# Kernel tuning notes

Hardware: AMD Instinct MI355X
Metric: run time of the kernel (lower is better)

The kernel has to match this reference:

```python
import jax, jax.numpy as jnp
import numpy as np

B, N, D, DB, C = 1024, 131072, 256, 512, 96


def setup_inputs() -> dict:
    key = jax.random.key(0)
    ks = jax.random.split(key, 9)
    s1 = 1.0 / np.sqrt(D)   # torch Linear default init bound for W1/b1
    s2 = 1.0 / np.sqrt(DB)  # for W2
    sl = 1.0 / np.sqrt(2.0) # custom init for label Linear(1, D)
    return {
        "x": jax.random.normal(ks[0], (B, D), jnp.float32),
        "k": jax.random.normal(ks[1], (B, D), jnp.float32),
        "candidate_k": jax.random.normal(ks[2], (N, D), jnp.float32),
        "candidate_y": jax.random.normal(ks[3], (N,), jnp.float32),
        "W_lbl": jax.random.uniform(ks[4], (D, 1), jnp.float32, -sl, sl),
        "b_lbl": jax.random.uniform(ks[5], (D,), jnp.float32, -sl, sl),
        "W1": jax.random.uniform(ks[6], (DB, D), jnp.float32, -s1, s1),
        "b1": jax.random.uniform(ks[7], (DB,), jnp.float32, -s1, s1),
        "W2": jax.random.uniform(ks[8], (D, DB), jnp.float32, -s2, s2),
        "context_size": C,
    }


def reference(x, k, candidate_k, candidate_y, W_lbl, b_lbl, W1, b1, W2, context_size):
    # --- exact L2 kNN search (FAISS IndexFlatL2 equivalent, eval path) ---
    # argmin_c ||k - c||^2 == argmax_c (2 k.c - ||c||^2); ||k||^2 is constant per row.
    neg_dist = 2.0 * (k @ candidate_k.T) - jnp.sum(candidate_k * candidate_k, axis=-1)[None, :]  # [B, N]
    _, context_idx = jax.lax.top_k(neg_dist, context_size)  # [B, C], non-differentiable (matches torch.no_grad)

    context_k = candidate_k[context_idx]  # [B, C, D]
    context_y = candidate_y[context_idx]  # [B, C]

    # similarities = -||k||^2 + 2 k.ck - ||ck||^2
    sim = (-jnp.sum(k * k, axis=-1, keepdims=True)
           + 2.0 * jnp.einsum('bd,bcd->bc', k, context_k)
           - jnp.sum(context_k * context_k, axis=-1))
    probs = jax.nn.softmax(sim, axis=-1)  # context_dropout=0 -> identity

    # label_encoder = Linear(1, D): y[..., None] @ W_lbl.T + b_lbl
    context_y_emb = context_y[..., None] * W_lbl[:, 0] + b_lbl  # [B, C, D]

    # T = Linear(D, DB) -> ReLU -> (dropout0=0) -> Linear(DB, D, bias=False)
    diff = k[:, None, :] - context_k                            # [B, C, D]
    h = jax.nn.relu(jnp.einsum('bcd,ed->bce', diff, W1) + b1)   # [B, C, DB]
    values = context_y_emb + jnp.einsum('bce,de->bcd', h, W2)   # [B, C, D]

    context_x = jnp.einsum('bc,bcd->bd', probs, values)
    return x + context_x
```

## Files before the change

kernel.cpp:

```cpp
#include <hip/hip_runtime.h>
#include <stdint.h>

#define B_   1024
#define N_   131072
#define D_   256
#define DB_  512
#define C_   96
#define CAP_ 2048

#define CHUNK_   4096
#define TILE_SH_ 32768

typedef __attribute__((ext_vector_type(8))) short bf16x8;
typedef __attribute__((ext_vector_type(4))) float f32x4;

__device__ __forceinline__ unsigned short f2bf(float x) {
  union { float f; unsigned u; } v; v.f = x;
  unsigned r = v.u + 0x7FFFu + ((v.u >> 16) & 1u);
  return (unsigned short)(r >> 16);
}
__device__ __forceinline__ float bf2f(unsigned short b) {
  union { unsigned u; float f; } v; v.u = ((unsigned)b) << 16;
  return v.f;
}

#if __has_builtin(__builtin_amdgcn_global_load_lds)
#define USE_ASYNC_LDS 1
#else
#define USE_ASYNC_LDS 0
#endif

__device__ __forceinline__ void stage_chunk(const unsigned short* chunk,
                                            unsigned short* lds, int t) {
#if USE_ASYNC_LDS
  char* base = (char*)lds + (t >> 6) * 1024;
  const unsigned short* g0 = chunk + t * 8;
  __builtin_amdgcn_global_load_lds((__attribute__((address_space(1))) void*)g0,
                                   (__attribute__((address_space(3))) void*)base, 16, 0, 0);
  __builtin_amdgcn_global_load_lds((__attribute__((address_space(1))) void*)(g0 + 2048),
                                   (__attribute__((address_space(3))) void*)(base + 4096), 16, 0, 0);
#else
  *(uint4*)((char*)lds + t * 16)        = *(const uint4*)(chunk + t * 8);
  *(uint4*)((char*)lds + t * 16 + 4096) = *(const uint4*)(chunk + t * 8 + 2048);
#endif
}

__global__ __launch_bounds__(256) void k_prep_cand(const float* __restrict__ cand,
                                                   unsigned short* __restrict__ cand_bf,
                                                   float* __restrict__ cnorm) {
  int w = threadIdx.x >> 6, l = threadIdx.x & 63;
  int row = blockIdx.x * 4 + w;
  float4 v = ((const float4*)(cand + (size_t)row * D_))[l];
  float s = v.x * v.x + v.y * v.y + v.z * v.z + v.w * v.w;
  ushort4 o = make_ushort4(f2bf(v.x), f2bf(v.y), f2bf(v.z), f2bf(v.w));
  int nt = row >> 7, r = row & 127;
  int kkc = l >> 3, cin = (l & 7) * 4;
  int c = (((cin >> 3) ^ ((r >> 1) & 3)) << 3) | (cin & 7);
  *(ushort4*)(cand_bf + ((size_t)nt * 8 + kkc) * CHUNK_ + r * 32 + c) = o;
  for (int off = 32; off; off >>= 1) s += __shfl_down(s, off);
  if (l == 0) cnorm[row] = s;
}

__global__ __launch_bounds__(256) void k_prep_k(const float* __restrict__ k,
                                                const float* __restrict__ W1,
                                                const float* __restrict__ b1,
                                                unsigned short* __restrict__ k_bf,
                                                float* __restrict__ knorm,
                                                float* __restrict__ tau,
                                                float* __restrict__ aprime) {
  __shared__ __align__(16) float kb[D_];
  __shared__ float red[4];
  int t = threadIdx.x, b = blockIdx.x;
  float kv = k[(size_t)b * D_ + t];
  kb[t] = kv;
  {
    int mt = b >> 7, r = b & 127;
    int kkc = t >> 5, cin = t & 31;
    int cb = (cin >> 3) ^ ((r >> 1) & 3);
    int c = (cb << 3) | (cin & 7);
    k_bf[((size_t)mt * 8 + kkc) * CHUNK_ + r * 32 + c] = f2bf(kv);
  }
  float p = kv * kv;
  for (int off = 32; off; off >>= 1) p += __shfl_down(p, off);
  if ((t & 63) == 0) red[t >> 6] = p;
  __syncthreads();
  if (t == 0) {
    float kn = red[0] + red[1] + red[2] + red[3];
    knorm[b] = kn;
    tau[b] = -256.0f + 2.5f * sqrtf(4.0f * kn + 512.0f);
  }
  for (int e = t; e < DB_; e += 256) {
    const float4* wr = (const float4*)(W1 + (size_t)e * D_);
    const float4* k4 = (const float4*)kb;
    float acc = 0.f;
    #pragma unroll 8
    for (int d = 0; d < D_ / 4; ++d) {
      float4 wv = wr[d], kv4 = k4[d];
      acc += wv.x * kv4.x + wv.y * kv4.y + wv.z * kv4.z + wv.w * kv4.w;
    }
    aprime[(size_t)b * DB_ + e] = acc + b1[e];
  }
}

__global__ __launch_bounds__(256) void k_prep_w1(const float* __restrict__ W1,
                                                 unsigned short* __restrict__ w1bf) {
  int i = blockIdx.x * 256 + threadIdx.x;
  float4 v = ((const float4*)W1)[i];
  int e = i >> 6, f4 = i & 63;
  int d0 = f4 * 4;
  int nt = e >> 7, r = e & 127;
  int kkc = d0 >> 5, cin = d0 & 31;
  int cb = (cin >> 3) ^ ((r >> 1) & 3);
  int c = (cb << 3) | (cin & 7);
  *(ushort4*)(w1bf + ((size_t)nt * 8 + kkc) * CHUNK_ + r * 32 + c) =
      make_ushort4(f2bf(v.x), f2bf(v.y), f2bf(v.z), f2bf(v.w));
}

__global__ __launch_bounds__(256, 2) void k_score(const unsigned short* __restrict__ k_bf,
                                                  const unsigned short* __restrict__ cand_bf,
                                                  const float* __restrict__ cnorm,
                                                  const float* __restrict__ tau,
                                                  unsigned* __restrict__ count,
                                                  int* __restrict__ l_idx,
                                                  float* __restrict__ l_s) {
  __shared__ __align__(16) unsigned short As[2][CHUNK_];
  __shared__ __align__(16) unsigned short Bs[2][CHUNK_];
  __shared__ float tauS[128], cnS[128];
  int t = threadIdx.x;
  unsigned x = blockIdx.x;
  unsigned xcd = x & 7u, j = x >> 3;
  int mt = (int)(j & 7u), nt = (int)(xcd + ((j >> 3) << 3));
  int m0 = mt * 128, n0 = nt * 128;
  const unsigned short* Ag = k_bf + (size_t)mt * TILE_SH_;
  const unsigned short* Bg = cand_bf + (size_t)nt * TILE_SH_;
  if (t < 128) tauS[t] = tau[m0 + t];
  if (t < 128) cnS[t] = cnorm[n0 + t];
  int lane = t & 63, w = t >> 6;
  int mb = (w & 1) * 64, nb = (w >> 1) * 64;
  int fr = lane & 15, fk = (lane >> 4) * 8;
  int fsw = fk ^ (((fr >> 1) & 3) << 3);
  f32x4 acc[4][4] = {};
  stage_chunk(Ag, As[0], t);
  stage_chunk(Bg, Bs[0], t);
  __syncthreads();
  #pragma unroll
  for (int kkc = 0; kkc < 8; ++kkc) {
    int cur = kkc & 1;
    if (kkc < 7) {
      stage_chunk(Ag + (kkc + 1) * CHUNK_, As[cur ^ 1], t);
      stage_chunk(Bg + (kkc + 1) * CHUNK_, Bs[cur ^ 1], t);
    }
    bf16x8 a[4], bq[4];
    #pragma unroll
    for (int i = 0; i < 4; ++i) a[i] = *(const bf16x8*)(As[cur] + (mb + i * 16 + fr) * 32 + fsw);
    #pragma unroll
    for (int jj = 0; jj < 4; ++jj) bq[jj] = *(const bf16x8*)(Bs[cur] + (nb + jj * 16 + fr) * 32 + fsw);
    #pragma unroll
    for (int i = 0; i < 4; ++i)
      #pragma unroll
      for (int jj = 0; jj < 4; ++jj)
        acc[i][jj] = __builtin_amdgcn_mfma_f32_16x16x32_bf16(a[i], bq[jj], acc[i][jj], 0, 0, 0);
    __syncthreads();
  }
  #pragma unroll
  for (int jj = 0; jj < 4; ++jj) {
    int nl = nb + jj * 16 + fr;
    float cn = cnS[nl];
    int ng = n0 + nl;
    #pragma unroll
    for (int i = 0; i < 4; ++i) {
      int mlb = mb + i * 16 + (lane >> 4) * 4;
      #pragma unroll
      for (int r = 0; r < 4; ++r) {
        float s = 2.0f * acc[i][jj][r] - cn;
        int ml = mlb + r;
        if (s > tauS[ml]) {
          int row = m0 + ml;
          unsigned pos = atomicAdd(&count[row], 1u);
          if (pos < CAP_) {
            l_idx[(size_t)row * CAP_ + pos] = ng;
            l_s[(size_t)row * CAP_ + pos] = s;
          }
        }
      }
    }
  }
}

__global__ __launch_bounds__(256, 2) void k_proj(const unsigned short* __restrict__ cand_bf,
                                                 const unsigned short* __restrict__ w1bf,
                                                 unsigned short* __restrict__ P) {
  __shared__ __align__(16) unsigned short As[2][CHUNK_];
  __shared__ __align__(16) unsigned short Bs[2][CHUNK_];
  int t = threadIdx.x;
  unsigned x = blockIdx.x;
  int mt = (int)(x >> 2), nt = (int)(x & 3u);
  int m0 = mt * 128, n0 = nt * 128;
  const unsigned short* Ag = cand_bf + (size_t)mt * TILE_SH_;
  const unsigned short* Bg = w1bf + (size_t)nt * TILE_SH_;
  int lane = t & 63, w = t >> 6;
  int mb = (w & 1) * 64, nb = (w >> 1) * 64;
  int fr = lane & 15, fk = (lane >> 4) * 8;
  int fsw = fk ^ (((fr >> 1) & 3) << 3);
  f32x4 acc[4][4] = {};
  stage_chunk(Ag, As[0], t);
  stage_chunk(Bg, Bs[0], t);
  __syncthreads();
  #pragma unroll
  for (int kkc = 0; kkc < 8; ++kkc) {
    int cur = kkc & 1;
    if (kkc < 7) {
      stage_chunk(Ag + (kkc + 1) * CHUNK_, As[cur ^ 1], t);
      stage_chunk(Bg + (kkc + 1) * CHUNK_, Bs[cur ^ 1], t);
    }
    bf16x8 a[4], bq[4];
    #pragma unroll
    for (int i = 0; i < 4; ++i) a[i] = *(const bf16x8*)(As[cur] + (mb + i * 16 + fr) * 32 + fsw);
    #pragma unroll
    for (int jj = 0; jj < 4; ++jj) bq[jj] = *(const bf16x8*)(Bs[cur] + (nb + jj * 16 + fr) * 32 + fsw);
    #pragma unroll
    for (int i = 0; i < 4; ++i)
      #pragma unroll
      for (int jj = 0; jj < 4; ++jj)
        acc[i][jj] = __builtin_amdgcn_mfma_f32_16x16x32_bf16(a[i], bq[jj], acc[i][jj], 0, 0, 0);
    __syncthreads();
  }
  #pragma unroll
  for (int jj = 0; jj < 4; ++jj) {
    int nl = nb + jj * 16 + fr;
    #pragma unroll
    for (int i = 0; i < 4; ++i) {
      int mlb = mb + i * 16 + (lane >> 4) * 4;
      #pragma unroll
      for (int r = 0; r < 4; ++r)
        P[(size_t)(m0 + mlb + r) * DB_ + n0 + nl] = f2bf(acc[i][jj][r]);
    }
  }
}

__global__ __launch_bounds__(256) void k_topk(const unsigned* __restrict__ count,
                                              const int* __restrict__ l_idx,
                                              const float* __restrict__ l_s,
                                              int* __restrict__ sel) {
  __shared__ unsigned keyS[CAP_];
  __shared__ int idxS[CAP_];
  __shared__ unsigned hist[256];
  __shared__ unsigned sca[256];
  __shared__ int bselS, needS;
  __shared__ int takenGT, takenEQ;
  int b = blockIdx.x, t = threadIdx.x;
  unsigned craw = count[b];
  int cnt = (int)(craw < (unsigned)CAP_ ? craw : (unsigned)CAP_);
  for (int i = t; i < cnt; i += 256) {
    unsigned u = __float_as_uint(l_s[(size_t)b * CAP_ + i]);
    u = (u & 0x80000000u) ? ~u : (u | 0x80000000u);
    keyS[i] = u;
    idxS[i] = l_idx[(size_t)b * CAP_ + i];
  }
  __syncthreads();
  if (cnt <= C_) {
    if (t < C_) sel[b * C_ + t] = (t < cnt) ? idxS[t] : t;
    return;
  }
  unsigned pref = 0;
  int need = C_;
  for (int shift = 24; shift >= 0; shift -= 8) {
    hist[t] = 0;
    __syncthreads();
    for (int i = t; i < cnt; i += 256) {
      unsigned u = keyS[i];
      bool in = (shift == 24) || ((u >> (shift + 8)) == (pref >> (shift + 8)));
      if (in) atomicAdd(&hist[(u >> shift) & 255u], 1u);
    }
    __syncthreads();
    sca[t] = hist[t];
    __syncthreads();
    for (int off = 1; off < 256; off <<= 1) {
      unsigned v = (t + off < 256) ? sca[t + off] : 0u;
      __syncthreads();
      sca[t] += v;
      __syncthreads();
    }
    if (t == 0) {
      int bk = 0;
      for (int jb = 255; jb >= 0; --jb)
        if (sca[jb] >= (unsigned)need) { bk = jb; break; }
      unsigned above = (bk < 255) ? sca[bk + 1] : 0u;
      bselS = bk;
      needS = need - (int)above;
      takenGT = 0;
      takenEQ = 0;
    }
    __syncthreads();
    pref |= ((unsigned)bselS) << shift;
    need = needS;
    __syncthreads();
  }
  int gtSlots = C_ - need;
  for (int i = t; i < cnt; i += 256) {
    unsigned u = keyS[i];
    if (u > pref) {
      int s_ = atomicAdd(&takenGT, 1);
      sel[b * C_ + s_] = idxS[i];
    } else if (u == pref) {
      int e = atomicAdd(&takenEQ, 1);
      if (e < need) sel[b * C_ + gtSlots + e] = idxS[i];
    }
  }
}

__global__ __launch_bounds__(256) void k_final(const float* __restrict__ x,
                                               const float* __restrict__ k,
                                               const float* __restrict__ cand,
                                               const float* __restrict__ candy,
                                               const float* __restrict__ Wl,
                                               const float* __restrict__ bl,
                                               const float* __restrict__ W2,
                                               const float* __restrict__ aprime,
                                               const float* __restrict__ cnorm,
                                               const float* __restrict__ knorm,
                                               const unsigned short* __restrict__ P,
                                               const int* __restrict__ sel,
                                               float* __restrict__ out) {
  __shared__ __align__(16) float kb[D_];
  __shared__ __align__(16) float a2[DB_];
  __shared__ __align__(16) float hbarS[DB_];
  __shared__ __align__(16) float hpart[4][DB_];
  __shared__ float sims[C_], yv[C_], probs[C_];
  __shared__ float red[128];
  __shared__ int selS[C_];
  int b = blockIdx.x, t = threadIdx.x, lane = t & 63, w = t >> 6;
  kb[t] = k[(size_t)b * D_ + t];
  a2[t] = aprime[(size_t)b * DB_ + t];
  a2[t + 256] = aprime[(size_t)b * DB_ + t + 256];
  if (t < C_) selS[t] = sel[b * C_ + t];
  __syncthreads();
  if (t < C_) yv[t] = candy[selS[t]];
  float kn = knorm[b];
  for (int c = w; c < C_; c += 4) {
    float4 cv = ((const float4*)(cand + (size_t)selS[c] * D_))[lane];
    float4 kv = ((const float4*)kb)[lane];
    float sp = kv.x * cv.x + kv.y * cv.y + kv.z * cv.z + kv.w * cv.w;
    for (int off = 32; off; off >>= 1) sp += __shfl_down(sp, off);
    if (lane == 0) sims[c] = -kn + 2.0f * sp - cnorm[selS[c]];
  }
  __syncthreads();
  if (t < 128) red[t] = (t < C_) ? sims[t] : -3.0e38f;
  __syncthreads();
  for (int off = 64; off >= 1; off >>= 1) {
    if (t < off) red[t] = fmaxf(red[t], red[t + off]);
    __syncthreads();
  }
  float mx = red[0];
  __syncthreads();
  if (t < C_) probs[t] = __expf(sims[t] - mx);
  __syncthreads();
  if (t < 128) red[t] = (t < C_) ? probs[t] : 0.f;
  __syncthreads();
  for (int off = 64; off >= 1; off >>= 1) {
    if (t < off) red[t] += red[t + off];
    __syncthreads();
  }
  float tot = red[0];
  __syncthreads();
  if (t < C_) probs[t] /= tot;
  __syncthreads();
  if (t < 128) red[t] = (t < C_) ? probs[t] * yv[t] : 0.f;
  __syncthreads();
  for (int off = 64; off >= 1; off >>= 1) {
    if (t < off) red[t] += red[t + off];
    __syncthreads();
  }
  float4 av0 = ((const float4*)a2)[lane];
  float4 av1 = ((const float4*)a2)[64 + lane];
  float h00 = 0, h01 = 0, h02 = 0, h03 = 0, h10 = 0, h11 = 0, h12 = 0, h13 = 0;
  for (int c = w; c < C_; c += 4) {
    float p = probs[c];
    const ushort4* pr = (const ushort4*)(P + (size_t)selS[c] * DB_);
    ushort4 u0 = pr[lane];
    ushort4 u1 = pr[64 + lane];
    h00 += p * fmaxf(av0.x - bf2f(u0.x), 0.f);
    h01 += p * fmaxf(av0.y - bf2f(u0.y), 0.f);
    h02 += p * fmaxf(av0.z - bf2f(u0.z), 0.f);
    h03 += p * fmaxf(av0.w - bf2f(u0.w), 0.f);
    h10 += p * fmaxf(av1.x - bf2f(u1.x), 0.f);
    h11 += p * fmaxf(av1.y - bf2f(u1.y), 0.f);
    h12 += p * fmaxf(av1.z - bf2f(u1.z), 0.f);
    h13 += p * fmaxf(av1.w - bf2f(u1.w), 0.f);
  }
  hpart[w][4 * lane + 0] = h00; hpart[w][4 * lane + 1] = h01;
  hpart[w][4 * lane + 2] = h02; hpart[w][4 * lane + 3] = h03;
  hpart[w][256 + 4 * lane + 0] = h10; hpart[w][256 + 4 * lane + 1] = h11;
  hpart[w][256 + 4 * lane + 2] = h12; hpart[w][256 + 4 * lane + 3] = h13;
  __syncthreads();
  hbarS[t] = hpart[0][t] + hpart[1][t] + hpart[2][t] + hpart[3][t];
  hbarS[t + 256] = hpart[0][t + 256] + hpart[1][t + 256] + hpart[2][t + 256] + hpart[3][t + 256];
  __syncthreads();
  float yb = red[0];
  const float4* w2r = (const float4*)(W2 + (size_t)t * DB_);
  const float4* hb4 = (const float4*)hbarS;
  float acc = 0.f;
  #pragma unroll 16
  for (int e = 0; e < DB_ / 4; ++e) {
    float4 wv = w2r[e], hv = hb4[e];
    acc += wv.x * hv.x + wv.y * hv.y + wv.z * hv.z + wv.w * hv.w;
  }
  float val = x[(size_t)b * D_ + t] + yb * Wl[t] + bl[t] + acc;
  out[(size_t)b * D_ + t] = val;
}

extern "C" void kernel_launch(void* const* d_in, const int* in_sizes, int n_in,
                              void* d_out, int out_size, void* d_ws, size_t ws_size,
                              hipStream_t stream) {
  const float* x     = (const float*)d_in[0];
  const float* k     = (const float*)d_in[1];
  const float* cand  = (const float*)d_in[2];
  const float* candy = (const float*)d_in[3];
  const float* Wl    = (const float*)d_in[4];
  const float* bl    = (const float*)d_in[5];
  const float* W1    = (const float*)d_in[6];
  const float* b1    = (const float*)d_in[7];
  const float* W2    = (const float*)d_in[8];

  char* ws = (char*)d_ws;
  unsigned short* candbf = (unsigned short*)(ws + 0);
  unsigned short* P      = (unsigned short*)(ws + 67108864);
  unsigned short* kbf    = (unsigned short*)(ws + 201326592);
  unsigned short* w1bf   = (unsigned short*)(ws + 201850880);
  float*          cnorm  = (float*)(ws + 202113024);
  float*          tau    = (float*)(ws + 202637312);
  float*          knorm  = (float*)(ws + 202641408);
  float*          aprime = (float*)(ws + 202645504);
  unsigned*       count  = (unsigned*)(ws + 204742656);
  int*            lidx   = (int*)(ws + 204746752);
  float*          ls     = (float*)(ws + 213135360);
  int*            sel    = (int*)(ws + 221523968);

  hipMemsetAsync(count, 0, B_ * sizeof(unsigned), stream);
  k_prep_cand<<<N_ / 4, 256, 0, stream>>>(cand, candbf, cnorm);
  k_prep_k<<<B_, 256, 0, stream>>>(k, W1, b1, kbf, knorm, tau, aprime);
  k_prep_w1<<<(DB_ * D_ / 4) / 256, 256, 0, stream>>>(W1, w1bf);
  k_score<<<(B_ / 128) * (N_ / 128), 256, 0, stream>>>(kbf, candbf, cnorm, tau, count, lidx, ls);
  k_proj<<<(N_ / 128) * (DB_ / 128), 256, 0, stream>>>(candbf, w1bf, P);
  k_topk<<<B_, 256, 0, stream>>>(count, lidx, ls, sel);
  k_final<<<B_, 256, 0, stream>>>(x, k, cand, candy, Wl, bl, W2, aprime, cnorm, knorm, P, sel,
                                  (float*)d_out);
}
```

Measured before the change: 670.8 us.

## Compute W1 projection only for selected neighbors inside final kernel

Removes the k_proj pass that projected all N candidates through W1 into a bf16 table P, and instead gathers the 96 selected candidates' bf16 rows into LDS in k_final and runs MFMA against W1 there, fusing ReLU and probability-weighted reduction. This avoids computing and writing projections for all 131072 candidates, of which only B*C rows are ever used. Separately, the per-row atomic counters are padded to a 16-word stride to reduce contention or false sharing in k_score. The final kernel now does more compute and uses a large LDS buffer, which may reduce occupancy.

```diff
diff --git a/kernel.cpp b/kernel.cpp
--- a/kernel.cpp
+++ b/kernel.cpp
@@ -7,6 +7,7 @@
 #define DB_  512
 #define C_   96
 #define CAP_ 2048
+#define CSTR 16
 
 #define CHUNK_   4096
 #define TILE_SH_ 32768
@@ -18,10 +19,6 @@
   union { float f; unsigned u; } v; v.f = x;
   unsigned r = v.u + 0x7FFFu + ((v.u >> 16) & 1u);
   return (unsigned short)(r >> 16);
-}
-__device__ __forceinline__ float bf2f(unsigned short b) {
-  union { unsigned u; float f; } v; v.u = ((unsigned)b) << 16;
-  return v.f;
 }
 
 #if __has_builtin(__builtin_amdgcn_global_load_lds)
@@ -176,64 +173,13 @@
         int ml = mlb + r;
         if (s > tauS[ml]) {
           int row = m0 + ml;
-          unsigned pos = atomicAdd(&count[row], 1u);
+          unsigned pos = atomicAdd(&count[(unsigned)row * CSTR], 1u);
           if (pos < CAP_) {
             l_idx[(size_t)row * CAP_ + pos] = ng;
             l_s[(size_t)row * CAP_ + pos] = s;
           }
         }
       }
-    }
-  }
-}
-
-__global__ __launch_bounds__(256, 2) void k_proj(const unsigned short* __restrict__ cand_bf,
-                                                 const unsigned short* __restrict__ w1bf,
-                                                 unsigned short* __restrict__ P) {
-  __shared__ __align__(16) unsigned short As[2][CHUNK_];
-  __shared__ __align__(16) unsigned short Bs[2][CHUNK_];
-  int t = threadIdx.x;
-  unsigned x = blockIdx.x;
-  int mt = (int)(x >> 2), nt = (int)(x & 3u);
-  int m0 = mt * 128, n0 = nt * 128;
-  const unsigned short* Ag = cand_bf + (size_t)mt * TILE_SH_;
-  const unsigned short* Bg = w1bf + (size_t)nt * TILE_SH_;
-  int lane = t & 63, w = t >> 6;
-  int mb = (w & 1) * 64, nb = (w >> 1) * 64;
-  int fr = lane & 15, fk = (lane >> 4) * 8;
-  int fsw = fk ^ (((fr >> 1) & 3) << 3);
-  f32x4 acc[4][4] = {};
-  stage_chunk(Ag, As[0], t);
-  stage_chunk(Bg, Bs[0], t);
-  __syncthreads();
-  #pragma unroll
-  for (int kkc = 0; kkc < 8; ++kkc) {
-    int cur = kkc & 1;
-    if (kkc < 7) {
-      stage_chunk(Ag + (kkc + 1) * CHUNK_, As[cur ^ 1], t);
-      stage_chunk(Bg + (kkc + 1) * CHUNK_, Bs[cur ^ 1], t);
-    }
-    bf16x8 a[4], bq[4];
-    #pragma unroll
-    for (int i = 0; i < 4; ++i) a[i] = *(const bf16x8*)(As[cur] + (mb + i * 16 + fr) * 32 + fsw);
-    #pragma unroll
-    for (int jj = 0; jj < 4; ++jj) bq[jj] = *(const bf16x8*)(Bs[cur] + (nb + jj * 16 + fr) * 32 + fsw);
-    #pragma unroll
-    for (int i = 0; i < 4; ++i)
-      #pragma unroll
-      for (int jj = 0; jj < 4; ++jj)
-        acc[i][jj] = __builtin_amdgcn_mfma_f32_16x16x32_bf16(a[i], bq[jj], acc[i][jj], 0, 0, 0);
-    __syncthreads();
-  }
-  #pragma unroll
-  for (int jj = 0; jj < 4; ++jj) {
-    int nl = nb + jj * 16 + fr;
-    #pragma unroll
-    for (int i = 0; i < 4; ++i) {
-      int mlb = mb + i * 16 + (lane >> 4) * 4;
-      #pragma unroll
-      for (int r = 0; r < 4; ++r)
-        P[(size_t)(m0 + mlb + r) * DB_ + n0 + nl] = f2bf(acc[i][jj][r]);
     }
   }
 }
@@ -249,7 +195,7 @@
   __shared__ int bselS, needS;
   __shared__ int takenGT, takenEQ;
   int b = blockIdx.x, t = threadIdx.x;
-  unsigned craw = count[b];
+  unsigned craw = count[(unsigned)b * CSTR];
   int cnt = (int)(craw < (unsigned)CAP_ ? craw : (unsigned)CAP_);
   for (int i = t; i < cnt; i += 256) {
     unsigned u = __float_as_uint(l_s[(size_t)b * CAP_ + i]);
@@ -319,13 +265,14 @@
                                                const float* __restrict__ aprime,
                                                const float* __restrict__ cnorm,
                                                const float* __restrict__ knorm,
-                                               const unsigned short* __restrict__ P,
+                                               const unsigned short* __restrict__ cand_bf,
+                                               const unsigned short* __restrict__ w1bf,
                                                const int* __restrict__ sel,
                                                float* __restrict__ out) {
+  __shared__ __align__(16) unsigned short Ash[8][96 * 32];
   __shared__ __align__(16) float kb[D_];
   __shared__ __align__(16) float a2[DB_];
   __shared__ __align__(16) float hbarS[DB_];
-  __shared__ __align__(16) float hpart[4][DB_];
   __shared__ float sims[C_], yv[C_], probs[C_];
   __shared__ float red[128];
   __shared__ int selS[C_];
@@ -336,6 +283,16 @@
   if (t < C_) selS[t] = sel[b * C_ + t];
   __syncthreads();
   if (t < C_) yv[t] = candy[selS[t]];
+  for (int u = t; u < 96 * 32; u += 256) {
+    int c = u >> 5, q = u & 31;
+    int kkc = q >> 2, sub = q & 3;
+    int sr = selS[c];
+    int ntg = sr >> 7, r = sr & 127;
+    int gsub = sub ^ ((r >> 1) & 3);
+    uint4 v = *(const uint4*)(cand_bf + ((size_t)ntg * 8 + kkc) * CHUNK_ + r * 32 + gsub * 8);
+    int lsub = sub ^ ((c >> 1) & 3);
+    *(uint4*)(&Ash[kkc][c * 32 + lsub * 8]) = v;
+  }
   float kn = knorm[b];
   for (int c = w; c < C_; c += 4) {
     float4 cv = ((const float4*)(cand + (size_t)selS[c] * D_))[lane];
@@ -371,41 +328,56 @@
     if (t < off) red[t] += red[t + off];
     __syncthreads();
   }
-  float4 av0 = ((const float4*)a2)[lane];
-  float4 av1 = ((const float4*)a2)[64 + lane];
-  float h00 = 0, h01 = 0, h02 = 0, h03 = 0, h10 = 0, h11 = 0, h12 = 0, h13 = 0;
-  for (int c = w; c < C_; c += 4) {
-    float p = probs[c];
-    const ushort4* pr = (const ushort4*)(P + (size_t)selS[c] * DB_);
-    ushort4 u0 = pr[lane];
-    ushort4 u1 = pr[64 + lane];
-    h00 += p * fmaxf(av0.x - bf2f(u0.x), 0.f);
-    h01 += p * fmaxf(av0.y - bf2f(u0.y), 0.f);
-    h02 += p * fmaxf(av0.z - bf2f(u0.z), 0.f);
-    h03 += p * fmaxf(av0.w - bf2f(u0.w), 0.f);
-    h10 += p * fmaxf(av1.x - bf2f(u1.x), 0.f);
-    h11 += p * fmaxf(av1.y - bf2f(u1.y), 0.f);
-    h12 += p * fmaxf(av1.z - bf2f(u1.z), 0.f);
-    h13 += p * fmaxf(av1.w - bf2f(u1.w), 0.f);
-  }
-  hpart[w][4 * lane + 0] = h00; hpart[w][4 * lane + 1] = h01;
-  hpart[w][4 * lane + 2] = h02; hpart[w][4 * lane + 3] = h03;
-  hpart[w][256 + 4 * lane + 0] = h10; hpart[w][256 + 4 * lane + 1] = h11;
-  hpart[w][256 + 4 * lane + 2] = h12; hpart[w][256 + 4 * lane + 3] = h13;
-  __syncthreads();
-  hbarS[t] = hpart[0][t] + hpart[1][t] + hpart[2][t] + hpart[3][t];
-  hbarS[t + 256] = hpart[0][t + 256] + hpart[1][t + 256] + hpart[2][t + 256] + hpart[3][t + 256];
+  int fr = lane & 15, fk = (lane >> 4) * 8, g4 = lane >> 4;
+  int fsw = fk ^ (((fr >> 1) & 3) << 3);
+  #pragma unroll
+  for (int hh = 0; hh < 2; ++hh) {
+    f32x4 acc[6][4] = {};
+    #pragma unroll
+    for (int kkc = 0; kkc < 8; ++kkc) {
+      bf16x8 a[6], bq[4];
+      #pragma unroll
+      for (int i = 0; i < 6; ++i)
+        a[i] = *(const bf16x8*)(&Ash[kkc][(i * 16 + fr) * 32 + fsw]);
+      #pragma unroll
+      for (int jj = 0; jj < 4; ++jj) {
+        int rw = hh * 64 + jj * 16 + fr;
+        bq[jj] = *(const bf16x8*)(w1bf + ((size_t)w * 8 + kkc) * CHUNK_ + rw * 32 + fsw);
+      }
+      #pragma unroll
+      for (int i = 0; i < 6; ++i)
+        #pragma unroll
+        for (int jj = 0; jj < 4; ++jj)
+          acc[i][jj] = __builtin_amdgcn_mfma_f32_16x16x32_bf16(a[i], bq[jj], acc[i][jj], 0, 0, 0);
+    }
+    #pragma unroll
+    for (int jj = 0; jj < 4; ++jj) {
+      int e = w * 128 + hh * 64 + jj * 16 + fr;
+      float ae = a2[e];
+      float hp = 0.f;
+      #pragma unroll
+      for (int i = 0; i < 6; ++i)
+        #pragma unroll
+        for (int r = 0; r < 4; ++r) {
+          int c = i * 16 + g4 * 4 + r;
+          hp += probs[c] * fmaxf(ae - acc[i][jj][r], 0.f);
+        }
+      hp += __shfl_xor(hp, 16);
+      hp += __shfl_xor(hp, 32);
+      if (g4 == 0) hbarS[e] = hp;
+    }
+  }
   __syncthreads();
   float yb = red[0];
   const float4* w2r = (const float4*)(W2 + (size_t)t * DB_);
   const float4* hb4 = (const float4*)hbarS;
-  float acc = 0.f;
+  float acc2 = 0.f;
   #pragma unroll 16
   for (int e = 0; e < DB_ / 4; ++e) {
     float4 wv = w2r[e], hv = hb4[e];
-    acc += wv.x * hv.x + wv.y * hv.y + wv.z * hv.z + wv.w * hv.w;
-  }
-  float val = x[(size_t)b * D_ + t] + yb * Wl[t] + bl[t] + acc;
+    acc2 += wv.x * hv.x + wv.y * hv.y + wv.z * hv.z + wv.w * hv.w;
+  }
+  float val = x[(size_t)b * D_ + t] + yb * Wl[t] + bl[t] + acc2;
   out[(size_t)b * D_ + t] = val;
 }
 
@@ -424,25 +396,23 @@
 
   char* ws = (char*)d_ws;
   unsigned short* candbf = (unsigned short*)(ws + 0);
-  unsigned short* P      = (unsigned short*)(ws + 67108864);
+  unsigned*       count  = (unsigned*)(ws + 67108864);
   unsigned short* kbf    = (unsigned short*)(ws + 201326592);
   unsigned short* w1bf   = (unsigned short*)(ws + 201850880);
   float*          cnorm  = (float*)(ws + 202113024);
   float*          tau    = (float*)(ws + 202637312);
   float*          knorm  = (float*)(ws + 202641408);
   float*          aprime = (float*)(ws + 202645504);
-  unsigned*       count  = (unsigned*)(ws + 204742656);
   int*            lidx   = (int*)(ws + 204746752);
   float*          ls     = (float*)(ws + 213135360);
   int*            sel    = (int*)(ws + 221523968);
 
-  hipMemsetAsync(count, 0, B_ * sizeof(unsigned), stream);
+  hipMemsetAsync(count, 0, B_ * CSTR * sizeof(unsigned), stream);
   k_prep_cand<<<N_ / 4, 256, 0, stream>>>(cand, candbf, cnorm);
   k_prep_k<<<B_, 256, 0, stream>>>(k, W1, b1, kbf, knorm, tau, aprime);
   k_prep_w1<<<(DB_ * D_ / 4) / 256, 256, 0, stream>>>(W1, w1bf);
   k_score<<<(B_ / 128) * (N_ / 128), 256, 0, stream>>>(kbf, candbf, cnorm, tau, count, lidx, ls);
-  k_proj<<<(N_ / 128) * (DB_ / 128), 256, 0, stream>>>(candbf, w1bf, P);
   k_topk<<<B_, 256, 0, stream>>>(count, lidx, ls, sel);
-  k_final<<<B_, 256, 0, stream>>>(x, k, cand, candy, Wl, bl, W2, aprime, cnorm, knorm, P, sel,
-                                  (float*)d_out);
-}
+  k_final<<<B_, 256, 0, stream>>>(x, k, cand, candy, Wl, bl, W2, aprime, cnorm, knorm,
+                                  candbf, w1bf, sel, (float*)d_out);
+}
```

Result: faster. 590.4 us (-12.0%).
